# Optimization experiments

Hardware: AMD Instinct MI355X
Metric: run time of the kernel (lower is better)

The kernel has to match this reference:

```python
import jax, jax.numpy as jnp
import numpy as np

B, S, HID = 1, 4096, 2048
NH, NKV, HD = 16, 4, 128
BLK, LOCAL, GLOB, STRIDE = 128, 4, 4, 8
NEG = -1e9


def _rotate_half(x):
    x1 = x[..., : x.shape[-1] // 2]
    x2 = x[..., x.shape[-1] // 2 :]
    return jnp.concatenate([-x2, x1], axis=-1)


def setup_inputs() -> dict:
    key = jax.random.key(0)
    ks = jax.random.split(key, 6)
    hidden_states = jax.random.normal(ks[0], (B, S, HID), jnp.float32)
    attention_mask_2d = jnp.ones((B, S), jnp.float32)
    # RoPE tables (b=1 broadcasts over batch, heads)
    pos = jnp.arange(S, dtype=jnp.float32)
    inv = 1.0 / (10000.0 ** (jnp.arange(0, HD, 2, dtype=jnp.float32) / HD))
    fr = pos[:, None] * inv[None, :]
    emb = jnp.concatenate([fr, fr], axis=-1)
    cos = jnp.cos(emb)[None]
    sin = jnp.sin(emb)[None]
    sc = 0.02
    Wq = jax.random.normal(ks[1], (HID, NH * HD), jnp.float32) * sc
    Wk = jax.random.normal(ks[2], (HID, NKV * HD), jnp.float32) * sc
    Wv = jax.random.normal(ks[3], (HID, NKV * HD), jnp.float32) * sc
    Wo = jax.random.normal(ks[4], (NH * HD, HID), jnp.float32) * sc
    return dict(hidden_states=hidden_states, attention_mask_2d=attention_mask_2d,
                cos=cos, sin=sin, Wq=Wq, Wk=Wk, Wv=Wv, Wo=Wo)


def reference(hidden_states, attention_mask_2d, cos, sin, Wq, Wk, Wv, Wo):
    b, Sq, _ = hidden_states.shape
    q = (hidden_states @ Wq).reshape(b, Sq, NH, HD).transpose(0, 2, 1, 3)
    k = (hidden_states @ Wk).reshape(b, Sq, NKV, HD).transpose(0, 2, 1, 3)
    v = (hidden_states @ Wv).reshape(b, Sq, NKV, HD).transpose(0, 2, 1, 3)
    c, s = cos[:, None], sin[:, None]  # broadcast over heads
    q = q * c + _rotate_half(q) * s
    k = k * c + _rotate_half(k) * s
    rep = NH // NKV
    k = jnp.repeat(k, rep, axis=1)
    v = jnp.repeat(v, rep, axis=1)

    scaling = HD ** -0.5
    N = Sq // BLK  # seq divisible by block_size -> pad=0 in the original
    qb = q.reshape(b, NH, N, BLK, HD).astype(jnp.float32)
    kb = k.reshape(b, NH, N, BLK, HD).astype(jnp.float32)
    vb = v.reshape(b, NH, N, BLK, HD).astype(jnp.float32)
    km = attention_mask_2d.reshape(b, N, BLK)

    # ---- local windows: LOCAL blocks ending at the current block ----
    Lp = LOCAL - 1
    kp = jnp.pad(kb, ((0, 0), (0, 0), (Lp, 0), (0, 0), (0, 0)))
    vp = jnp.pad(vb, ((0, 0), (0, 0), (Lp, 0), (0, 0), (0, 0)))
    kmp = jnp.pad(km, ((0, 0), (Lp, 0), (0, 0)))  # padded blocks masked (0)
    win = jnp.arange(N)[:, None] + jnp.arange(LOCAL)[None, :]  # (N, LOCAL)
    k_local = kp[:, :, win]          # (b,h,N,LOCAL,BLK,HD)
    v_local = vp[:, :, win]
    km_local = kmp[:, win]           # (b,N,LOCAL,BLK)

    s_local = jnp.einsum('bhntd,bhnlsd->bhntls', qb, k_local) * scaling
    s_local = s_local + (1.0 - km_local)[:, None, :, None, :, :] * NEG
    intra = jnp.triu(jnp.full((BLK, BLK), NEG, jnp.float32), 1)  # causal inside current block only
    s_local = s_local.at[:, :, :, :, -1, :].add(intra)
    s_local = s_local.reshape(b, NH, N, BLK, LOCAL * BLK)

    # ---- global blocks: block 0 + strided past blocks, dedup -> masked ----
    i = jnp.arange(N)
    offsets = jnp.arange(GLOB - 1, 0, -1) * STRIDE
    idx = jnp.clip(i[:, None] - offsets[None, :], 0)
    idx = jnp.concatenate([jnp.zeros((N, 1), idx.dtype), idx], axis=1)  # (N, GLOB)
    dup = idx[:, 1:] == idx[:, :-1]
    g_valid = jnp.concatenate([jnp.ones((N, 1), bool), ~dup], axis=1).astype(jnp.float32)
    k_g = kb[:, :, idx]              # (b,h,N,GLOB,BLK,HD) gather of global blocks
    v_g = vb[:, :, idx]
    km_g = km[:, idx] * g_valid[None, :, :, None]  # (b,N,GLOB,BLK)

    s_g = jnp.einsum('bhntd,bhngsd->bhntgs', qb, k_g) * scaling
    s_g = s_g + (1.0 - km_g)[:, None, :, None, :, :] * NEG
    s_g = s_g.reshape(b, NH, N, BLK, GLOB * BLK)

    scores = jnp.concatenate([s_local, s_g], axis=-1)  # (b,h,N,BLK,(LOCAL+GLOB)*BLK)
    v_all = jnp.concatenate([v_local.reshape(b, NH, N, LOCAL * BLK, HD),
                             v_g.reshape(b, NH, N, GLOB * BLK, HD)], axis=-2)
    probs = jax.nn.softmax(scores, axis=-1)  # dropout_p = 0 (eval)
    out = jnp.einsum('bhntk,bhnkd->bhntd', probs, v_all)
    out = out.reshape(b, NH, Sq, HD).transpose(0, 2, 1, 3).reshape(b, Sq, NH * HD)
    return out @ Wo
```

## Files before the change

### kernel.cpp

```cpp
#include <hip/hip_runtime.h>
#include <hip/hip_bf16.h>
#include <cstdint>

#define NEGV   (-1000000000.0f)
#define SCALE  0.08838834764831845f

typedef __bf16 bf16x8 __attribute__((ext_vector_type(8)));
typedef float  f32x4  __attribute__((ext_vector_type(4)));
typedef unsigned short u16;
typedef unsigned int   u32;

#define MFMA16(a, b, c) __builtin_amdgcn_mfma_f32_16x16x32_bf16((a), (b), (c), 0, 0, 0)

#define WS_XP    ((size_t)0)
#define WS_AOP   ((size_t)0)
#define WS_WQP   ((size_t)8388608)
#define WS_WKP   ((size_t)12582912)
#define WS_WVP   ((size_t)13631488)
#define WS_WOP   ((size_t)14680064)
#define WS_QF    ((size_t)18874368)
#define WS_KF    ((size_t)27262976)
#define WS_VF    ((size_t)29360128)

__device__ __forceinline__ u16 f2bf(float f) {
  union { float f; u32 u; } v; v.f = f;
  u32 u = v.u;
  u += 0x7FFFu + ((u >> 16) & 1u);
  return (u16)(u >> 16);
}

__device__ __forceinline__ void gl_lds16(const u16* g, u16* l) {
  __builtin_amdgcn_global_load_lds((const __attribute__((address_space(1))) u32*)g,
                                   (__attribute__((address_space(3))) u32*)l,
                                   16, 0, 0);
}

__device__ __forceinline__ int fragoff(int row, int k) {
  return ((row >> 4) * 64 + ((k >> 3) & 3) * 16 + (row & 15)) * 8 + (k & 7);
}

__global__ __launch_bounds__(256, 4)
void convert_kernel(const float* __restrict__ X,
                    const float* __restrict__ Wq,
                    const float* __restrict__ Wk,
                    const float* __restrict__ Wv,
                    const float* __restrict__ Wo,
                    u16* __restrict__ ws)
{
  const int t = blockIdx.x;
  const int tid = threadIdx.x;
  const float* src; u16* dst; int tt, ldn; bool amode = false;
  if (t < 2048)      { src = X;  dst = ws + WS_XP;  tt = t;        ldn = 2048; amode = true; }
  else if (t < 3072) { src = Wq; dst = ws + WS_WQP; tt = t - 2048; ldn = 2048; }
  else if (t < 3328) { src = Wk; dst = ws + WS_WKP; tt = t - 3072; ldn = 512;  }
  else if (t < 3584) { src = Wv; dst = ws + WS_WVP; tt = t - 3328; ldn = 512;  }
  else               { src = Wo; dst = ws + WS_WOP; tt = t - 3584; ldn = 2048; }
  const int rb = tt >> 6, kb = tt & 63;
  #pragma unroll
  for (int p = 0; p < 2; ++p) {
    const int c = tid + 256 * p;
    const int row = (c >> 6) * 16 + (c & 15);
    const int k0  = ((c >> 4) & 3) * 8;
    union { u16 h[8]; uint4 v; } pk;
    if (amode) {
      const float* s0 = src + (size_t)(rb * 128 + row) * 2048 + kb * 32 + k0;
      const float4 a0 = *reinterpret_cast<const float4*>(s0);
      const float4 a1 = *reinterpret_cast<const float4*>(s0 + 4);
      pk.h[0] = f2bf(a0.x); pk.h[1] = f2bf(a0.y); pk.h[2] = f2bf(a0.z); pk.h[3] = f2bf(a0.w);
      pk.h[4] = f2bf(a1.x); pk.h[5] = f2bf(a1.y); pk.h[6] = f2bf(a1.z); pk.h[7] = f2bf(a1.w);
    } else {
      #pragma unroll
      for (int j = 0; j < 8; ++j)
        pk.h[j] = f2bf(src[(size_t)(kb * 32 + k0 + j) * ldn + rb * 128 + row]);
    }
    *reinterpret_cast<uint4*>(dst + (size_t)tt * 4096 + c * 8) = pk.v;
  }
}

__device__ __forceinline__ void gemm_core(const u16* __restrict__ pa,
                                          const u16* __restrict__ pb,
                                          u16* As, u16* Bs,
                                          int tid, int wave, int lane,
                                          f32x4 acc[2][8])
{
  for (int it = 0; it < 64; ++it) {
    __syncthreads();
    gl_lds16(pa + tid * 8,         As + tid * 8);
    gl_lds16(pa + (tid + 256) * 8, As + (tid + 256) * 8);
    gl_lds16(pb + tid * 8,         Bs + tid * 8);
    gl_lds16(pb + (tid + 256) * 8, Bs + (tid + 256) * 8);
    pa += 4096; pb += 4096;
    __syncthreads();
    bf16x8 af0 = *reinterpret_cast<const bf16x8*>(As + (wave * 2 + 0) * 512 + lane * 8);
    bf16x8 af1 = *reinterpret_cast<const bf16x8*>(As + (wave * 2 + 1) * 512 + lane * 8);
    #pragma unroll
    for (int nt = 0; nt < 8; ++nt) {
      const bf16x8 bfr = *reinterpret_cast<const bf16x8*>(Bs + nt * 512 + lane * 8);
      acc[0][nt] = MFMA16(af0, bfr, acc[0][nt]);
      acc[1][nt] = MFMA16(af1, bfr, acc[1][nt]);
    }
  }
}

__global__ __launch_bounds__(256, 2)
void qkv_kernel(const float* __restrict__ cosp,
                const float* __restrict__ sinp,
                u16* __restrict__ ws)
{
  const int mb = blockIdx.x, bn = blockIdx.y;
  const int tid = threadIdx.x;
  const int wave = tid >> 6, lane = tid & 63;
  const int lq = lane >> 4, l16 = lane & 15;

  const u16* Ab = ws + WS_XP + (size_t)mb * 64 * 4096;
  const u16* Bb; int seg, hh;
  if (bn < 16)      { Bb = ws + WS_WQP + (size_t)bn * 64 * 4096;        seg = 0; hh = bn; }
  else if (bn < 20) { Bb = ws + WS_WKP + (size_t)(bn - 16) * 64 * 4096; seg = 1; hh = bn - 16; }
  else              { Bb = ws + WS_WVP + (size_t)(bn - 20) * 64 * 4096; seg = 2; hh = bn - 20; }

  __shared__ __align__(16) u16 As[4096];
  __shared__ __align__(16) u16 Bs[4096];

  f32x4 acc[2][8];
  #pragma unroll
  for (int i = 0; i < 2; ++i)
    #pragma unroll
    for (int j = 0; j < 8; ++j)
      #pragma unroll
      for (int r = 0; r < 4; ++r) acc[i][j][r] = 0.0f;

  gemm_core(Ab, Bb, As, Bs, tid, wave, lane, acc);

  const int m0 = mb * 128;
  if (seg == 2) {
    u16* V = ws + WS_VF + (size_t)hh * 524288;
    #pragma unroll
    for (int mt = 0; mt < 2; ++mt)
      #pragma unroll
      for (int nt = 0; nt < 8; ++nt) {
        const int d = nt * 16 + l16;
        #pragma unroll
        for (int r = 0; r < 4; ++r) {
          const int s = m0 + wave * 32 + mt * 16 + lq * 4 + r;
          V[(s >> 5) * 4096 + fragoff(d, s & 31)] = f2bf(acc[mt][nt][r]);
        }
      }
  } else {
    u16* D = ws + ((seg == 0) ? WS_QF : WS_KF) + (size_t)hh * 524288;
    #pragma unroll
    for (int mt = 0; mt < 2; ++mt)
      #pragma unroll
      for (int r = 0; r < 4; ++r) {
        const int s = m0 + wave * 32 + mt * 16 + lq * 4 + r;
        const int sl = s & 127;
        u16* Dt = D + (size_t)(s >> 7) * 4 * 4096;
        #pragma unroll
        for (int nt = 0; nt < 4; ++nt) {
          const int d1 = nt * 16 + l16, d2 = d1 + 64;
          const float c  = cosp[s * 128 + d1];
          const float sn = sinp[s * 128 + d1];
          const float v1 = acc[mt][nt][r], v2 = acc[mt][nt + 4][r];
          Dt[(d1 >> 5) * 4096 + fragoff(sl, d1 & 31)] = f2bf(v1 * c - v2 * sn);
          Dt[(d2 >> 5) * 4096 + fragoff(sl, d2 & 31)] = f2bf(v2 * c + v1 * sn);
        }
      }
  }
}

__global__ __launch_bounds__(256, 2)
void attn_kernel(const float* __restrict__ amask, u16* __restrict__ ws)
{
  const int n = blockIdx.x, h = blockIdx.y;
  const int kvh = h >> 2;
  const int tid = threadIdx.x;
  const int wave = tid >> 6, lane = tid & 63;
  const int lq = lane >> 4, l16 = lane & 15;

  const u16* Kfb = ws + WS_KF + (size_t)kvh * 524288;
  const u16* Vfb = ws + WS_VF + (size_t)kvh * 524288;
  u16* AOp = ws + WS_AOP;

  __shared__ __align__(16) u16 bufK[16384];
  __shared__ __align__(16) u16 bufV[16384];

  const u16* Qb = ws + WS_QF + (size_t)h * 524288 + (size_t)n * 4 * 4096;
  bf16x8 qf[2][4];
  #pragma unroll
  for (int mt = 0; mt < 2; ++mt)
    #pragma unroll
    for (int kk = 0; kk < 4; ++kk)
      qf[mt][kk] = *reinterpret_cast<const bf16x8*>(
          Qb + (size_t)kk * 4096 + ((wave * 2 + mt) * 64 + lane) * 8);

  f32x4 O[2][8];
  #pragma unroll
  for (int i = 0; i < 2; ++i)
    #pragma unroll
    for (int j = 0; j < 8; ++j)
      #pragma unroll
      for (int r = 0; r < 4; ++r) O[i][j][r] = 0.0f;
  float mrow[2][4], lrow[2][4];
  #pragma unroll
  for (int i = 0; i < 2; ++i)
    #pragma unroll
    for (int r = 0; r < 4; ++r) { mrow[i][r] = -3.0e38f; lrow[i][r] = 0.0f; }

  int gidx[4]; bool gval[4];
  gidx[0] = 0;
  gidx[1] = (n - 24 > 0) ? n - 24 : 0;
  gidx[2] = (n - 16 > 0) ? n - 16 : 0;
  gidx[3] = (n - 8  > 0) ? n - 8  : 0;
  gval[0] = true;
  gval[1] = (gidx[1] != gidx[0]);
  gval[2] = (gidx[2] != gidx[1]);
  gval[3] = (gidx[3] != gidx[2]);

  for (int kb = 0; kb < 8; ++kb) {
    int bkey; bool bvalid; bool intra;
    if (kb < 4) { bkey = n - 3 + kb; bvalid = (bkey >= 0); intra = (kb == 3); }
    else        { bkey = gidx[kb - 4]; bvalid = gval[kb - 4]; intra = false; }
    const int bload = bvalid ? bkey : 0;

    const u16* Kb = Kfb + (size_t)bload * 16384;
    const u16* Vb = Vfb + (size_t)bload * 16384;
    __syncthreads();
    #pragma unroll
    for (int p = 0; p < 8; ++p) {
      gl_lds16(Kb + (tid + 256 * p) * 8, bufK + (tid + 256 * p) * 8);
      gl_lds16(Vb + (tid + 256 * p) * 8, bufV + (tid + 256 * p) * 8);
    }
    __syncthreads();

    f32x4 sacc[2][8];
    #pragma unroll
    for (int i = 0; i < 2; ++i)
      #pragma unroll
      for (int j = 0; j < 8; ++j)
        #pragma unroll
        for (int r = 0; r < 4; ++r) sacc[i][j][r] = 0.0f;
    #pragma unroll
    for (int kk = 0; kk < 4; ++kk)
      #pragma unroll
      for (int nt = 0; nt < 8; ++nt) {
        const bf16x8 bfr = *reinterpret_cast<const bf16x8*>(
            bufK + ((kk * 8 + nt) * 64 + lane) * 8);
        sacc[0][nt] = MFMA16(qf[0][kk], bfr, sacc[0][nt]);
        sacc[1][nt] = MFMA16(qf[1][kk], bfr, sacc[1][nt]);
      }

    float kmv[8];
    #pragma unroll
    for (int nt = 0; nt < 8; ++nt)
      kmv[nt] = bvalid ? amask[bload * 128 + nt * 16 + l16] : 0.0f;

    __syncthreads();

    u16* pw = bufK + wave * 4096;
    #pragma unroll
    for (int mt = 0; mt < 2; ++mt)
      #pragma unroll
      for (int r = 0; r < 4; ++r) {
        const int tq = wave * 32 + mt * 16 + lq * 4 + r;
        float sv[8];
        float rmax = -3.0e38f;
        #pragma unroll
        for (int nt = 0; nt < 8; ++nt) {
          float s = sacc[mt][nt][r] * SCALE + (1.0f - kmv[nt]) * NEGV;
          const int tk = nt * 16 + l16;
          if (intra && tk > tq) s += NEGV;
          sv[nt] = s;
          rmax = fmaxf(rmax, s);
        }
        #pragma unroll
        for (int off = 1; off < 16; off <<= 1)
          rmax = fmaxf(rmax, __shfl_xor(rmax, off, 64));
        const float mold = mrow[mt][r];
        const float mnew = fmaxf(mold, rmax);
        const float alpha = __expf(mold - mnew);
        float rsum = 0.0f;
        u16 pb[8];
        #pragma unroll
        for (int nt = 0; nt < 8; ++nt) {
          const float pe = __expf(sv[nt] - mnew);
          rsum += pe;
          pb[nt] = f2bf(pe);
        }
        #pragma unroll
        for (int off = 1; off < 16; off <<= 1)
          rsum += __shfl_xor(rsum, off, 64);
        lrow[mt][r] = lrow[mt][r] * alpha + rsum;
        mrow[mt][r] = mnew;
        #pragma unroll
        for (int nt = 0; nt < 8; ++nt) O[mt][nt][r] *= alpha;
        const int l8 = l16 >> 3;
        #pragma unroll
        for (int nt = 0; nt < 8; ++nt) {
          const int lqp = (nt * 2 + l8) & 3;
          pw[(nt >> 1) * 1024 + ((mt * 4 + lqp) * 16 + lq * 4 + r) * 8 + (l16 & 7)] = pb[nt];
        }
      }

    #pragma unroll
    for (int kk = 0; kk < 4; ++kk) {
      const bf16x8 pf0 = *reinterpret_cast<const bf16x8*>(pw + kk * 1024 + lane * 8);
      const bf16x8 pf1 = *reinterpret_cast<const bf16x8*>(pw + kk * 1024 + (64 + lane) * 8);
      #pragma unroll
      for (int nt = 0; nt < 8; ++nt) {
        const bf16x8 vfr = *reinterpret_cast<const bf16x8*>(
            bufV + ((kk * 8 + nt) * 64 + lane) * 8);
        O[0][nt] = MFMA16(pf0, vfr, O[0][nt]);
        O[1][nt] = MFMA16(pf1, vfr, O[1][nt]);
      }
    }
  }

  #pragma unroll
  for (int mt = 0; mt < 2; ++mt)
    #pragma unroll
    for (int r = 0; r < 4; ++r) {
      const float inv = 1.0f / lrow[mt][r];
      const int s = n * 128 + wave * 32 + mt * 16 + lq * 4 + r;
      #pragma unroll
      for (int nt = 0; nt < 8; ++nt) {
        const int kcol = h * 128 + nt * 16 + l16;
        AOp[((size_t)(s >> 7) * 64 + (kcol >> 5)) * 4096 + fragoff(s & 127, kcol & 31)] =
            f2bf(O[mt][nt][r] * inv);
      }
    }
}

__global__ __launch_bounds__(256, 2)
void outproj_kernel(const u16* __restrict__ ws, float* __restrict__ Out)
{
  const int mb = blockIdx.x, bn = blockIdx.y;
  const int tid = threadIdx.x;
  const int wave = tid >> 6, lane = tid & 63;
  const int lq = lane >> 4, l16 = lane & 15;

  const u16* Ab = ws + WS_AOP + (size_t)mb * 64 * 4096;
  const u16* Bb = ws + WS_WOP + (size_t)bn * 64 * 4096;

  __shared__ __align__(16) u16 As[4096];
  __shared__ __align__(16) u16 Bs[4096];

  f32x4 acc[2][8];
  #pragma unroll
  for (int i = 0; i < 2; ++i)
    #pragma unroll
    for (int j = 0; j < 8; ++j)
      #pragma unroll
      for (int r = 0; r < 4; ++r) acc[i][j][r] = 0.0f;

  gemm_core(Ab, Bb, (u16*)As, (u16*)Bs, tid, wave, lane, acc);

  #pragma unroll
  for (int mt = 0; mt < 2; ++mt)
    #pragma unroll
    for (int nt = 0; nt < 8; ++nt) {
      const int ccol = bn * 128 + nt * 16 + l16;
      #pragma unroll
      for (int r = 0; r < 4; ++r) {
        const int s = mb * 128 + wave * 32 + mt * 16 + lq * 4 + r;
        Out[(size_t)s * 2048 + ccol] = acc[mt][nt][r];
      }
    }
}

extern "C" void kernel_launch(void* const* d_in, const int* in_sizes, int n_in,
                              void* d_out, int out_size, void* d_ws, size_t ws_size,
                              hipStream_t stream) {
  const float* X     = (const float*)d_in[0];
  const float* amask = (const float*)d_in[1];
  const float* cosp  = (const float*)d_in[2];
  const float* sinp  = (const float*)d_in[3];
  const float* Wq    = (const float*)d_in[4];
  const float* Wk    = (const float*)d_in[5];
  const float* Wv    = (const float*)d_in[6];
  const float* Wo    = (const float*)d_in[7];
  float* Out = (float*)d_out;
  u16* ws = (u16*)d_ws;

  hipLaunchKernelGGL(convert_kernel, dim3(4608), dim3(256), 0, stream,
                     X, Wq, Wk, Wv, Wo, ws);
  hipLaunchKernelGGL(qkv_kernel, dim3(32, 24), dim3(256), 0, stream,
                     cosp, sinp, ws);
  hipLaunchKernelGGL(attn_kernel, dim3(32, 16), dim3(256), 0, stream,
                     amask, ws);
  hipLaunchKernelGGL(outproj_kernel, dim3(32, 16), dim3(256), 0, stream,
                     ws, Out);
}
```

Before: 302.3 us.

## Stage weight transpose through LDS, skip invalid key blocks, use 8-wave attention blocks

The weight conversion now reads rows with coalesced float4 loads into a shared tile and then transposes from LDS, replacing strided scalar global reads. The attention kernel moves from 4 waves handling 32 query rows each to 8 waves handling 16 rows each, which halves per-thread accumulator registers and raises occupancy. It also skips key blocks that are out of range or duplicate global blocks instead of loading and masking them. The trade-off is more blocks and barriers per block, plus a branchy loop that now varies in length per block.

Measured after the change: 293.0 us. 3.1% less time.

```diff
diff --git a/kernel.cpp b/kernel.cpp
--- a/kernel.cpp
+++ b/kernel.cpp
@@ -56,24 +56,43 @@
   else if (t < 3584) { src = Wv; dst = ws + WS_WVP; tt = t - 3328; ldn = 512;  }
   else               { src = Wo; dst = ws + WS_WOP; tt = t - 3584; ldn = 2048; }
   const int rb = tt >> 6, kb = tt & 63;
-  #pragma unroll
-  for (int p = 0; p < 2; ++p) {
-    const int c = tid + 256 * p;
-    const int row = (c >> 6) * 16 + (c & 15);
-    const int k0  = ((c >> 4) & 3) * 8;
-    union { u16 h[8]; uint4 v; } pk;
-    if (amode) {
+
+  if (amode) {
+    #pragma unroll
+    for (int p = 0; p < 2; ++p) {
+      const int c = tid + 256 * p;
+      const int row = (c >> 6) * 16 + (c & 15);
+      const int k0  = ((c >> 4) & 3) * 8;
+      union { u16 h[8]; uint4 v; } pk;
       const float* s0 = src + (size_t)(rb * 128 + row) * 2048 + kb * 32 + k0;
       const float4 a0 = *reinterpret_cast<const float4*>(s0);
       const float4 a1 = *reinterpret_cast<const float4*>(s0 + 4);
       pk.h[0] = f2bf(a0.x); pk.h[1] = f2bf(a0.y); pk.h[2] = f2bf(a0.z); pk.h[3] = f2bf(a0.w);
       pk.h[4] = f2bf(a1.x); pk.h[5] = f2bf(a1.y); pk.h[6] = f2bf(a1.z); pk.h[7] = f2bf(a1.w);
-    } else {
-      #pragma unroll
-      for (int j = 0; j < 8; ++j)
-        pk.h[j] = f2bf(src[(size_t)(kb * 32 + k0 + j) * ldn + rb * 128 + row]);
-    }
-    *reinterpret_cast<uint4*>(dst + (size_t)tt * 4096 + c * 8) = pk.v;
+      *reinterpret_cast<uint4*>(dst + (size_t)tt * 4096 + c * 8) = pk.v;
+    }
+  } else {
+    __shared__ u16 Ls[32][136];
+    #pragma unroll
+    for (int i = 0; i < 4; ++i) {
+      const int c = tid + 256 * i;
+      const int k = c >> 5, n4 = c & 31;
+      const float4 wv = *reinterpret_cast<const float4*>(
+          src + (size_t)(kb * 32 + k) * ldn + rb * 128 + n4 * 4);
+      u16* d = &Ls[k][n4 * 4];
+      d[0] = f2bf(wv.x); d[1] = f2bf(wv.y); d[2] = f2bf(wv.z); d[3] = f2bf(wv.w);
+    }
+    __syncthreads();
+    #pragma unroll
+    for (int p = 0; p < 2; ++p) {
+      const int c = tid + 256 * p;
+      const int row = (c >> 6) * 16 + (c & 15);
+      const int k0  = ((c >> 4) & 3) * 8;
+      union { u16 h[8]; uint4 v; } pk;
+      #pragma unroll
+      for (int j = 0; j < 8; ++j) pk.h[j] = Ls[k0 + j][row];
+      *reinterpret_cast<uint4*>(dst + (size_t)tt * 4096 + c * 8) = pk.v;
+    }
   }
 }
 
@@ -153,7 +172,7 @@
       for (int r = 0; r < 4; ++r) {
         const int s = m0 + wave * 32 + mt * 16 + lq * 4 + r;
         const int sl = s & 127;
-        u16* Dt = D + (size_t)(s >> 7) * 4 * 4096;
+        u16* Dt = D + (size_t)(s >> 7) * 16384;
         #pragma unroll
         for (int nt = 0; nt < 4; ++nt) {
           const int d1 = nt * 16 + l16, d2 = d1 + 64;
@@ -167,7 +186,7 @@
   }
 }
 
-__global__ __launch_bounds__(256, 2)
+__global__ __launch_bounds__(512, 4)
 void attn_kernel(const float* __restrict__ amask, u16* __restrict__ ws)
 {
   const int n = blockIdx.x, h = blockIdx.y;
@@ -183,27 +202,20 @@
   __shared__ __align__(16) u16 bufK[16384];
   __shared__ __align__(16) u16 bufV[16384];
 
-  const u16* Qb = ws + WS_QF + (size_t)h * 524288 + (size_t)n * 4 * 4096;
-  bf16x8 qf[2][4];
-  #pragma unroll
-  for (int mt = 0; mt < 2; ++mt)
-    #pragma unroll
-    for (int kk = 0; kk < 4; ++kk)
-      qf[mt][kk] = *reinterpret_cast<const bf16x8*>(
-          Qb + (size_t)kk * 4096 + ((wave * 2 + mt) * 64 + lane) * 8);
-
-  f32x4 O[2][8];
-  #pragma unroll
-  for (int i = 0; i < 2; ++i)
-    #pragma unroll
-    for (int j = 0; j < 8; ++j)
-      #pragma unroll
-      for (int r = 0; r < 4; ++r) O[i][j][r] = 0.0f;
-  float mrow[2][4], lrow[2][4];
-  #pragma unroll
-  for (int i = 0; i < 2; ++i)
-    #pragma unroll
-    for (int r = 0; r < 4; ++r) { mrow[i][r] = -3.0e38f; lrow[i][r] = 0.0f; }
+  const u16* Qb = ws + WS_QF + (size_t)h * 524288 + (size_t)n * 16384;
+  bf16x8 qf[4];
+  #pragma unroll
+  for (int kk = 0; kk < 4; ++kk)
+    qf[kk] = *reinterpret_cast<const bf16x8*>(Qb + (size_t)kk * 4096 + (wave * 64 + lane) * 8);
+
+  f32x4 O[8];
+  #pragma unroll
+  for (int j = 0; j < 8; ++j)
+    #pragma unroll
+    for (int r = 0; r < 4; ++r) O[j][r] = 0.0f;
+  float mrow[4], lrow[4];
+  #pragma unroll
+  for (int r = 0; r < 4; ++r) { mrow[r] = -3.0e38f; lrow[r] = 0.0f; }
 
   int gidx[4]; bool gval[4];
   gidx[0] = 0;
@@ -219,114 +231,102 @@
     int bkey; bool bvalid; bool intra;
     if (kb < 4) { bkey = n - 3 + kb; bvalid = (bkey >= 0); intra = (kb == 3); }
     else        { bkey = gidx[kb - 4]; bvalid = gval[kb - 4]; intra = false; }
-    const int bload = bvalid ? bkey : 0;
-
-    const u16* Kb = Kfb + (size_t)bload * 16384;
-    const u16* Vb = Vfb + (size_t)bload * 16384;
-    __syncthreads();
-    #pragma unroll
-    for (int p = 0; p < 8; ++p) {
-      gl_lds16(Kb + (tid + 256 * p) * 8, bufK + (tid + 256 * p) * 8);
-      gl_lds16(Vb + (tid + 256 * p) * 8, bufV + (tid + 256 * p) * 8);
-    }
-    __syncthreads();
-
-    f32x4 sacc[2][8];
-    #pragma unroll
-    for (int i = 0; i < 2; ++i)
-      #pragma unroll
-      for (int j = 0; j < 8; ++j)
-        #pragma unroll
-        for (int r = 0; r < 4; ++r) sacc[i][j][r] = 0.0f;
+    if (!bvalid) continue;
+
+    const u16* Kb = Kfb + (size_t)bkey * 16384;
+    const u16* Vb = Vfb + (size_t)bkey * 16384;
+    __syncthreads();
+    #pragma unroll
+    for (int p = 0; p < 4; ++p) {
+      gl_lds16(Kb + (tid + 512 * p) * 8, bufK + (tid + 512 * p) * 8);
+      gl_lds16(Vb + (tid + 512 * p) * 8, bufV + (tid + 512 * p) * 8);
+    }
+    __syncthreads();
+
+    f32x4 sacc[8];
+    #pragma unroll
+    for (int j = 0; j < 8; ++j)
+      #pragma unroll
+      for (int r = 0; r < 4; ++r) sacc[j][r] = 0.0f;
     #pragma unroll
     for (int kk = 0; kk < 4; ++kk)
       #pragma unroll
       for (int nt = 0; nt < 8; ++nt) {
         const bf16x8 bfr = *reinterpret_cast<const bf16x8*>(
             bufK + ((kk * 8 + nt) * 64 + lane) * 8);
-        sacc[0][nt] = MFMA16(qf[0][kk], bfr, sacc[0][nt]);
-        sacc[1][nt] = MFMA16(qf[1][kk], bfr, sacc[1][nt]);
+        sacc[nt] = MFMA16(qf[kk], bfr, sacc[nt]);
       }
 
     float kmv[8];
     #pragma unroll
     for (int nt = 0; nt < 8; ++nt)
-      kmv[nt] = bvalid ? amask[bload * 128 + nt * 16 + l16] : 0.0f;
-
-    __syncthreads();
-
-    u16* pw = bufK + wave * 4096;
-    #pragma unroll
-    for (int mt = 0; mt < 2; ++mt)
-      #pragma unroll
-      for (int r = 0; r < 4; ++r) {
-        const int tq = wave * 32 + mt * 16 + lq * 4 + r;
-        float sv[8];
-        float rmax = -3.0e38f;
-        #pragma unroll
-        for (int nt = 0; nt < 8; ++nt) {
-          float s = sacc[mt][nt][r] * SCALE + (1.0f - kmv[nt]) * NEGV;
-          const int tk = nt * 16 + l16;
-          if (intra && tk > tq) s += NEGV;
-          sv[nt] = s;
-          rmax = fmaxf(rmax, s);
-        }
-        #pragma unroll
-        for (int off = 1; off < 16; off <<= 1)
-          rmax = fmaxf(rmax, __shfl_xor(rmax, off, 64));
-        const float mold = mrow[mt][r];
-        const float mnew = fmaxf(mold, rmax);
-        const float alpha = __expf(mold - mnew);
-        float rsum = 0.0f;
-        u16 pb[8];
-        #pragma unroll
-        for (int nt = 0; nt < 8; ++nt) {
-          const float pe = __expf(sv[nt] - mnew);
-          rsum += pe;
-          pb[nt] = f2bf(pe);
-        }
-        #pragma unroll
-        for (int off = 1; off < 16; off <<= 1)
-          rsum += __shfl_xor(rsum, off, 64);
-        lrow[mt][r] = lrow[mt][r] * alpha + rsum;
-        mrow[mt][r] = mnew;
-        #pragma unroll
-        for (int nt = 0; nt < 8; ++nt) O[mt][nt][r] *= alpha;
-        const int l8 = l16 >> 3;
-        #pragma unroll
-        for (int nt = 0; nt < 8; ++nt) {
-          const int lqp = (nt * 2 + l8) & 3;
-          pw[(nt >> 1) * 1024 + ((mt * 4 + lqp) * 16 + lq * 4 + r) * 8 + (l16 & 7)] = pb[nt];
-        }
-      }
+      kmv[nt] = amask[bkey * 128 + nt * 16 + l16];
+
+    __syncthreads();
+
+    u16* pw = bufK + wave * 2048;
+    #pragma unroll
+    for (int r = 0; r < 4; ++r) {
+      const int tq = wave * 16 + lq * 4 + r;
+      float sv[8];
+      float rmax = -3.0e38f;
+      #pragma unroll
+      for (int nt = 0; nt < 8; ++nt) {
+        float s = sacc[nt][r] * SCALE + (1.0f - kmv[nt]) * NEGV;
+        const int tk = nt * 16 + l16;
+        if (intra && tk > tq) s += NEGV;
+        sv[nt] = s;
+        rmax = fmaxf(rmax, s);
+      }
+      #pragma unroll
+      for (int off = 1; off < 16; off <<= 1)
+        rmax = fmaxf(rmax, __shfl_xor(rmax, off, 64));
+      const float mold = mrow[r];
+      const float mnew = fmaxf(mold, rmax);
+      const float alpha = __expf(mold - mnew);
+      float rsum = 0.0f;
+      u16 pb[8];
+      #pragma unroll
+      for (int nt = 0; nt < 8; ++nt) {
+        const float pe = __expf(sv[nt] - mnew);
+        rsum += pe;
+        pb[nt] = f2bf(pe);
+      }
+      #pragma unroll
+      for (int off = 1; off < 16; off <<= 1)
+        rsum += __shfl_xor(rsum, off, 64);
+      lrow[r] = lrow[r] * alpha + rsum;
+      mrow[r] = mnew;
+      #pragma unroll
+      for (int nt = 0; nt < 8; ++nt) O[nt][r] *= alpha;
+      #pragma unroll
+      for (int nt = 0; nt < 8; ++nt)
+        pw[(nt >> 1) * 512 + ((((nt & 1) * 2 + (l16 >> 3)) * 16) + lq * 4 + r) * 8 + (l16 & 7)] = pb[nt];
+    }
 
     #pragma unroll
     for (int kk = 0; kk < 4; ++kk) {
-      const bf16x8 pf0 = *reinterpret_cast<const bf16x8*>(pw + kk * 1024 + lane * 8);
-      const bf16x8 pf1 = *reinterpret_cast<const bf16x8*>(pw + kk * 1024 + (64 + lane) * 8);
+      const bf16x8 pf = *reinterpret_cast<const bf16x8*>(pw + kk * 512 + lane * 8);
       #pragma unroll
       for (int nt = 0; nt < 8; ++nt) {
         const bf16x8 vfr = *reinterpret_cast<const bf16x8*>(
             bufV + ((kk * 8 + nt) * 64 + lane) * 8);
-        O[0][nt] = MFMA16(pf0, vfr, O[0][nt]);
-        O[1][nt] = MFMA16(pf1, vfr, O[1][nt]);
-      }
-    }
-  }
-
-  #pragma unroll
-  for (int mt = 0; mt < 2; ++mt)
-    #pragma unroll
-    for (int r = 0; r < 4; ++r) {
-      const float inv = 1.0f / lrow[mt][r];
-      const int s = n * 128 + wave * 32 + mt * 16 + lq * 4 + r;
-      #pragma unroll
-      for (int nt = 0; nt < 8; ++nt) {
-        const int kcol = h * 128 + nt * 16 + l16;
-        AOp[((size_t)(s >> 7) * 64 + (kcol >> 5)) * 4096 + fragoff(s & 127, kcol & 31)] =
-            f2bf(O[mt][nt][r] * inv);
-      }
-    }
+        O[nt] = MFMA16(pf, vfr, O[nt]);
+      }
+    }
+  }
+
+  #pragma unroll
+  for (int r = 0; r < 4; ++r) {
+    const float inv = 1.0f / lrow[r];
+    const int s = n * 128 + wave * 16 + lq * 4 + r;
+    #pragma unroll
+    for (int nt = 0; nt < 8; ++nt) {
+      const int kcol = h * 128 + nt * 16 + l16;
+      AOp[((size_t)(s >> 7) * 64 + (kcol >> 5)) * 4096 + fragoff(s & 127, kcol & 31)] =
+          f2bf(O[nt][r] * inv);
+    }
+  }
 }
 
 __global__ __launch_bounds__(256, 2)
@@ -384,7 +384,7 @@
                      X, Wq, Wk, Wv, Wo, ws);
   hipLaunchKernelGGL(qkv_kernel, dim3(32, 24), dim3(256), 0, stream,
                      cosp, sinp, ws);
-  hipLaunchKernelGGL(attn_kernel, dim3(32, 16), dim3(256), 0, stream,
+  hipLaunchKernelGGL(attn_kernel, dim3(32, 16), dim3(512), 0, stream,
                      amask, ws);
   hipLaunchKernelGGL(outproj_kernel, dim3(32, 16), dim3(256), 0, stream,
                      ws, Out);
```
